# Performance work log

Measured on AMD Instinct MI355X. Metric: run time of the kernel, lower is better.

## Reference

```python
import jax, jax.numpy as jnp
import numpy as np

# LIFParameters(thr=0.4, tau=20.0, tau_o=20.0, damp=0.3, n_ref=5)
THR = 0.4
DECAY = float(np.exp(-1.0 / 20.0))   # membrane decay
KAPPA = float(np.exp(-1.0 / 20.0))   # output filter decay
N_REF = 5.0
DAMP = 0.3
SCALE = 1.0                           # scaling_factor

B, NIN, H, NOUT = 1024, 2048, 2048, 512


def setup_inputs() -> dict:
    key = jax.random.key(0)
    ks = jax.random.split(key, 10)
    inputs = (jax.random.uniform(ks[0], (B, NIN)) < 0.1).astype(jnp.float32)   # input spikes
    v = jax.random.uniform(ks[1], (B, H)) * THR                                # membrane potentials
    z = (jax.random.uniform(ks[2], (B, H)) < 0.2).astype(jnp.float32)          # previous spikes
    r = jax.random.randint(ks[3], (B, H), 0, 6).astype(jnp.float32)            # refractory counters
    out = jax.random.normal(ks[4], (B, NOUT)) * 0.1                            # filtered output
    trace_in = jax.random.uniform(ks[5], (B, NIN))
    trace_rec = jax.random.uniform(ks[6], (B, H))
    w_in = jax.random.normal(ks[7], (NIN, H)) / np.sqrt(NIN)
    w_rec = jax.random.normal(ks[8], (H, H)) / np.sqrt(H)
    w_out = jax.random.normal(ks[9], (H, NOUT)) / np.sqrt(H)
    return dict(inputs=inputs, v=v, z=z, r=r, out=out, trace_in=trace_in,
                trace_rec=trace_rec, w_in=w_in, w_rec=w_rec, w_out=w_out)


@jax.custom_vjp
def spike(v_scaled):
    return (v_scaled > 0.0).astype(v_scaled.dtype)

def _spike_fwd(v_scaled):
    return spike(v_scaled), v_scaled

def _spike_bwd(v_scaled, g):
    # surrogate gradient: damp * max(0, 1 - |v_scaled|)
    return (g * DAMP * jnp.maximum(1.0 - jnp.abs(v_scaled), 0.0),)

spike.defvjp(_spike_fwd, _spike_bwd)


def reference(inputs, v, z, r, out, trace_in, trace_rec, w_in, w_rec, w_out):
    # --- lif_step ---
    i_t = inputs @ w_in + z @ w_rec                      # [B,H] synaptic current
    new_v = DECAY * v + i_t - z * THR                    # leaky integration + reset
    v_scaled = (new_v - THR) / THR
    new_z = spike(v_scaled)
    new_z = jnp.where(r > 0.1, 0.0, new_z)               # refractory masking (old r)
    new_r = jnp.clip(r + N_REF * new_z - 1.0, 0.0, N_REF)
    new_out = KAPPA * out + new_z @ (w_out * SCALE)      # [B,NOUT]
    # --- e-prop extras (call_eprop) ---
    dz_dh = jnp.maximum(DAMP * (1.0 - jnp.abs(v_scaled)), 0.0) / THR
    dz_dh = jnp.where(r > 0.1, 0.0, dz_dh)               # zero in refractory period
    new_trace_in = trace_in * DECAY + inputs
    new_trace_rec = trace_rec * DECAY + z
    return (new_out, new_z, new_v, new_r, new_trace_in, new_trace_rec, dz_dh)
```

## Files before the change

### kernel.cpp

```cpp
#include <hip/hip_runtime.h>

#define Bq 1024
#define Hq 2048
#define NOUTq 512

#define DECAYF 0.95122942450071400910f
#define THRF 0.4f

#define OFF_OUT  0
#define OFF_Z    524288
#define OFF_V    2621440
#define OFF_R    4718592
#define OFF_TIN  6815744
#define OFF_TREC 8912896
#define OFF_DZ   11010048

#define WS_ACOMB 0ul
#define WS_WHI   8388608ul
#define WS_WLO   25165824ul
#define WS_WOUTT 41943040ul
#define WS_P     44040192ul
#define WS_Z2    77594624ul
#define WS_NEED  81788928ul

typedef __attribute__((ext_vector_type(8))) short  bf16x8;
typedef __attribute__((ext_vector_type(4))) short  s16x4;
typedef __attribute__((ext_vector_type(4))) float  f32x4;

__device__ __forceinline__ unsigned short cvt_bf16(float f) {
  unsigned u = __float_as_uint(f);
  return (unsigned short)((u + 0x7FFFu + ((u >> 16) & 1u)) >> 16);
}

__device__ __forceinline__ void gl_lds16(const void* g, void* l) {
  __builtin_amdgcn_global_load_lds((const __attribute__((address_space(1))) unsigned int*)g,
                                   (__attribute__((address_space(3))) unsigned int*)l, 16, 0, 0);
}


__global__ __launch_bounds__(256)
void prepWA(const float* __restrict__ w_in, const float* __restrict__ w_rec,
            const float* __restrict__ w_out, short* __restrict__ Whi,
            short* __restrict__ Wlo, short* __restrict__ WoutT,
            const f32x4* __restrict__ ins, const f32x4* __restrict__ zin,
            short* __restrict__ Acomb)
{
  __shared__ float tile[64][65];
  const int bx = blockIdx.x, tid = threadIdx.x;
  if (bx >= 2304) {
    const int i = (bx - 2304) * 256 + tid;
    const f32x4 b = ins[i];
    const f32x4 d = zin[i];
    const int e = i * 4, m = e >> 11, k = e & 2047;
    s16x4 ab, zb;
#pragma unroll
    for (int j = 0; j < 4; ++j) { ab[j] = (short)cvt_bf16(b[j]); zb[j] = (short)cvt_bf16(d[j]); }
    *(s16x4*)&Acomb[m * 4096 + k] = ab;
    *(s16x4*)&Acomb[m * 4096 + 2048 + k] = zb;
    return;
  }
  const int rr = tid >> 4, c4 = (tid & 15) * 4;
  if (bx < 2048) {
    const int k0 = (bx >> 5) * 64, n0 = (bx & 31) * 64;
#pragma unroll
    for (int p = 0; p < 4; ++p) {
      const int kk = p * 16 + rr, kg = k0 + kk;
      const float* src = (kg < 2048) ? &w_in[kg * 2048 + n0 + c4]
                                     : &w_rec[(kg - 2048) * 2048 + n0 + c4];
      const f32x4 v = *(const f32x4*)src;
#pragma unroll
      for (int j = 0; j < 4; ++j) tile[kk][c4 + j] = v[j];
    }
    __syncthreads();
#pragma unroll
    for (int p = 0; p < 4; ++p) {
      const int nn = p * 16 + rr;
      s16x4 hh, ll;
#pragma unroll
      for (int j = 0; j < 4; ++j) {
        const float w = tile[c4 + j][nn];
        const unsigned short h = cvt_bf16(w);
        hh[j] = (short)h;
        ll[j] = (short)cvt_bf16(w - __uint_as_float(((unsigned)h) << 16));
      }
      *(s16x4*)&Whi[(n0 + nn) * 4096 + k0 + c4] = hh;
      *(s16x4*)&Wlo[(n0 + nn) * 4096 + k0 + c4] = ll;
    }
  } else {
    const int b2 = bx - 2048;
    const int k0 = (b2 >> 3) * 64, n0 = (b2 & 7) * 64;
#pragma unroll
    for (int p = 0; p < 4; ++p) {
      const int kk = p * 16 + rr;
      const f32x4 v = *(const f32x4*)&w_out[(k0 + kk) * 512 + n0 + c4];
#pragma unroll
      for (int j = 0; j < 4; ++j) tile[kk][c4 + j] = v[j];
    }
    __syncthreads();
#pragma unroll
    for (int p = 0; p < 4; ++p) {
      const int nn = p * 16 + rr;
      s16x4 hh;
#pragma unroll
      for (int j = 0; j < 4; ++j) hh[j] = (short)cvt_bf16(tile[c4 + j][nn]);
      *(s16x4*)&WoutT[(n0 + nn) * 2048 + k0 + c4] = hh;
    }
  }
}

__global__ __launch_bounds__(256, 1)
void gemm1(const short* __restrict__ Ag, const short* __restrict__ Whg,
           const short* __restrict__ Wlg, float* __restrict__ outp)
{
  constexpr int BM = 128, BN = 128, MR = 4, NR = 4, KT = 16, AK = 4096;
  constexpr int APW = BM / 32, WPW = BN / 32;

  __shared__ __align__(16) short As[BM * 64];
  __shared__ __align__(16) short Wh[BN * 64];
  __shared__ __align__(16) short Wl[BN * 64];

  const int tid = threadIdx.x, lane = tid & 63, wv = tid >> 6;
  const int lr = lane & 15, hl = lane >> 4;
  const int rA = lane >> 3, ts = lane & 7;

  const int bid = blockIdx.x;
  const int swz = (bid & 7) * 64 + (bid >> 3);
  const int m0 = (swz & 7) * BM;
  const int n0 = ((swz >> 3) & 15) * BN;
  const int kz = swz >> 7;
  const int kb = kz * 1024;
  float* P = outp + (size_t)kz * (Bq * Hq);

  const int wm = (wv >> 1) * (MR * 16);
  const int wn = (wv & 1) * (NR * 16);

  f32x4 acc[MR][NR];
#pragma unroll
  for (int mi = 0; mi < MR; ++mi)
#pragma unroll
    for (int ni = 0; ni < NR; ++ni) acc[mi][ni] = (f32x4){0.f, 0.f, 0.f, 0.f};

  auto STAGE = [&](int kt) {
    const int k = kb + kt * 64;
#pragma unroll
    for (int q = 0; q < APW; ++q) {
      const int slot = wv * APW + q;
      const int r = slot * 8 + rA;
      const int s = ts ^ (r & 7);
      gl_lds16(Ag + (m0 + r) * AK + k + s * 8, &As[slot * 512]);
    }
#pragma unroll
    for (int q = 0; q < WPW; ++q) {
      const int slot = wv * WPW + q;
      const int r = slot * 8 + rA;
      const int s = ts ^ (r & 7);
      gl_lds16(Whg + (n0 + r) * AK + k + s * 8, &Wh[slot * 512]);
      gl_lds16(Wlg + (n0 + r) * AK + k + s * 8, &Wl[slot * 512]);
    }
  };

  STAGE(0);
  for (int kt = 0; kt < KT; ++kt) {
    __syncthreads();
#pragma unroll
    for (int ks = 0; ks < 2; ++ks) {
      bf16x8 af[MR];
#pragma unroll
      for (int mi = 0; mi < MR; ++mi) {
        const int r = wm + mi * 16 + lr;
        af[mi] = *(const bf16x8*)&As[r * 64 + (((ks * 4 + hl) ^ (r & 7)) << 3)];
      }
#pragma unroll
      for (int ni = 0; ni < NR; ++ni) {
        const int rn = wn + ni * 16 + lr;
        const int sp = (((ks * 4 + hl) ^ (rn & 7)) << 3);
        const bf16x8 bh = *(const bf16x8*)&Wh[rn * 64 + sp];
#pragma unroll
        for (int mi = 0; mi < MR; ++mi)
          acc[mi][ni] = __builtin_amdgcn_mfma_f32_16x16x32_bf16(af[mi], bh, acc[mi][ni], 0, 0, 0);
        const bf16x8 bl = *(const bf16x8*)&Wl[rn * 64 + sp];
#pragma unroll
        for (int mi = 0; mi < MR; ++mi)
          acc[mi][ni] = __builtin_amdgcn_mfma_f32_16x16x32_bf16(af[mi], bl, acc[mi][ni], 0, 0, 0);
      }
    }
    __syncthreads();
    if (kt + 1 < KT) STAGE(kt + 1);
  }

#pragma unroll
  for (int mi = 0; mi < MR; ++mi)
#pragma unroll
    for (int ni = 0; ni < NR; ++ni)
#pragma unroll
      for (int j = 0; j < 4; ++j) {
        const int m = m0 + wm + mi * 16 + hl * 4 + j;
        const int n = n0 + wn + ni * 16 + lr;
        P[m * Hq + n] = acc[mi][ni][j];
      }
}

__global__ __launch_bounds__(256)
void lif_epi(const f32x4* __restrict__ Pp, const f32x4* __restrict__ vin,
             const f32x4* __restrict__ zin, const f32x4* __restrict__ rin,
             float* __restrict__ dout, short* __restrict__ z2)
{
  const int i = blockIdx.x * 256 + threadIdx.x;
  const f32x4 it = Pp[i] + Pp[i + 524288] + Pp[i + 2 * 524288] + Pp[i + 3 * 524288];
  const f32x4 vo = vin[i], zo = zin[i], ro = rin[i];
  f32x4 nv, nz, nr, dz;
  s16x4 zb;
#pragma unroll
  for (int j = 0; j < 4; ++j) {
    const float v1 = DECAYF * vo[j] + it[j] - zo[j] * THRF;
    const float vs = (v1 - THRF) / THRF;
    const bool refr = ro[j] > 0.1f;
    const float z1 = (refr || !(vs > 0.0f)) ? 0.0f : 1.0f;
    nv[j] = v1; nz[j] = z1;
    nr[j] = fminf(fmaxf(ro[j] + 5.0f * z1 - 1.0f, 0.0f), 5.0f);
    dz[j] = refr ? 0.0f : (fmaxf(0.3f * (1.0f - fabsf(vs)), 0.0f) / THRF);
    zb[j] = (short)cvt_bf16(z1);
  }
  ((f32x4*)(dout + OFF_V))[i] = nv;
  ((f32x4*)(dout + OFF_Z))[i] = nz;
  ((f32x4*)(dout + OFF_R))[i] = nr;
  ((f32x4*)(dout + OFF_DZ))[i] = dz;
  ((s16x4*)z2)[i] = zb;
}

__global__ __launch_bounds__(256)
void tail(const short* __restrict__ Ag, const short* __restrict__ Whg,
          const float* __restrict__ e0, float* __restrict__ outp,
          const f32x4* __restrict__ tin, const f32x4* __restrict__ ins,
          const f32x4* __restrict__ trec, const f32x4* __restrict__ zin,
          f32x4* __restrict__ o1, f32x4* __restrict__ o2)
{
  constexpr int BM = 32, BN = 64, MR = 1, NR = 2, KT = 32, AK = 2048;
  constexpr int APW = BM / 32, WPW = BN / 32;
  __shared__ __align__(16) short As[BM * 64];
  __shared__ __align__(16) short Wh[BN * 64];

  const int bid = blockIdx.x, tid = threadIdx.x;
  if (bid >= 256) {
    const int i = (bid - 256) * 256 + tid;
    o1[i] = tin[i] * DECAYF + ins[i];
    o2[i] = trec[i] * DECAYF + zin[i];
    return;
  }
  const int lane = tid & 63, wv = tid >> 6;
  const int lr = lane & 15, hl = lane >> 4;
  const int rA = lane >> 3, ts = lane & 7;
  const int m0 = (bid >> 3) * BM, n0 = (bid & 7) * BN;
  const int wm = (wv >> 1) * (MR * 16);
  const int wn = (wv & 1) * (NR * 16);

  f32x4 acc[MR][NR];
#pragma unroll
  for (int mi = 0; mi < MR; ++mi)
#pragma unroll
    for (int ni = 0; ni < NR; ++ni) acc[mi][ni] = (f32x4){0.f, 0.f, 0.f, 0.f};

  auto STAGE = [&](int kt) {
    const int k = kt * 64;
#pragma unroll
    for (int q = 0; q < APW; ++q) {
      const int slot = wv * APW + q;
      const int r = slot * 8 + rA;
      const int s = ts ^ (r & 7);
      gl_lds16(Ag + (m0 + r) * AK + k + s * 8, &As[slot * 512]);
    }
#pragma unroll
    for (int q = 0; q < WPW; ++q) {
      const int slot = wv * WPW + q;
      const int r = slot * 8 + rA;
      const int s = ts ^ (r & 7);
      gl_lds16(Whg + (n0 + r) * AK + k + s * 8, &Wh[slot * 512]);
    }
  };

  STAGE(0);
  for (int kt = 0; kt < KT; ++kt) {
    __syncthreads();
#pragma unroll
    for (int ks = 0; ks < 2; ++ks) {
      bf16x8 af[MR];
#pragma unroll
      for (int mi = 0; mi < MR; ++mi) {
        const int r = wm + mi * 16 + lr;
        af[mi] = *(const bf16x8*)&As[r * 64 + (((ks * 4 + hl) ^ (r & 7)) << 3)];
      }
#pragma unroll
      for (int ni = 0; ni < NR; ++ni) {
        const int rn = wn + ni * 16 + lr;
        const int sp = (((ks * 4 + hl) ^ (rn & 7)) << 3);
        const bf16x8 bh = *(const bf16x8*)&Wh[rn * 64 + sp];
#pragma unroll
        for (int mi = 0; mi < MR; ++mi)
          acc[mi][ni] = __builtin_amdgcn_mfma_f32_16x16x32_bf16(af[mi], bh, acc[mi][ni], 0, 0, 0);
      }
    }
    __syncthreads();
    if (kt + 1 < KT) STAGE(kt + 1);
  }

#pragma unroll
  for (int mi = 0; mi < MR; ++mi)
#pragma unroll
    for (int ni = 0; ni < NR; ++ni)
#pragma unroll
      for (int j = 0; j < 4; ++j) {
        const int m = m0 + wm + mi * 16 + hl * 4 + j;
        const int n = n0 + wn + ni * 16 + lr;
        const int idx = m * NOUTq + n;
        outp[idx] = DECAYF * e0[idx] + acc[mi][ni][j];
      }
}


template<int MODE>
__global__ __launch_bounds__(256, 1)
void fb_gemm(const float* __restrict__ A0g, const float* __restrict__ A1g,
             const float* __restrict__ W0g, const float* __restrict__ W1g,
             const float* __restrict__ e0, const float* __restrict__ e1,
             const float* __restrict__ e2, float* __restrict__ dout)
{
  constexpr int BM = (MODE == 0) ? 64 : 32;
  constexpr int BN = (MODE == 0) ? 128 : 64;
  constexpr int BK = 64;
  constexpr int LDA = BK + 8;
  constexpr int MR = (MODE == 0) ? 2 : 1;
  constexpr int NR = (MODE == 0) ? 4 : 2;
  constexpr int WM = MR * 16, WN = NR * 16;
  constexpr int KT = (MODE == 0) ? 64 : 32;
  constexpr int Nmat = (MODE == 0) ? Hq : NOUTq;
  constexpr int QA = BM / 16;
  constexpr int QW = (16 * BN) / 256;
  constexpr int KSH = (MODE == 0) ? 7 : 6;
  constexpr int KSTEP = (MODE == 0) ? 2 : 4;

  __shared__ __align__(16) short As[BM * LDA];
  __shared__ __align__(16) short Wh[BN * LDA];
  __shared__ __align__(16) short Wl[((MODE == 0) ? BN : 1) * LDA];

  const int tid  = threadIdx.x;
  const int lane = tid & 63;
  const int wave = tid >> 6;
  const int lr = lane & 15, hl = lane >> 4;
  const int wmOff = (wave >> 1) * WM;
  const int wnOff = (wave & 1) * WN;
  const int m0 = blockIdx.y * BM;
  const int n0 = blockIdx.x * BN;
  const int arow = tid >> 4, ac4 = tid & 15;
  const int wn = tid & (BN - 1);

  f32x4 aR[QA];
  float wR[QW][4];
  f32x4 acc[MR][NR];
#pragma unroll
  for (int mi = 0; mi < MR; ++mi)
#pragma unroll
    for (int ni = 0; ni < NR; ++ni)
      acc[mi][ni] = (f32x4){0.f, 0.f, 0.f, 0.f};

  auto LOAD = [&](int kt) {
    const float* Ag = A0g; const float* Wg = W0g; int k0 = kt * BK;
    if (MODE == 0 && kt >= 32) { Ag = A1g; Wg = W1g; k0 = (kt - 32) * BK; }
#pragma unroll
    for (int q = 0; q < QA; ++q)
      aR[q] = *(const f32x4*)&Ag[(m0 + arow + q * 16) * 2048 + k0 + ac4 * 4];
#pragma unroll
    for (int p = 0; p < QW; ++p) {
      const int kq = (tid >> KSH) + p * KSTEP;
#pragma unroll
      for (int i = 0; i < 4; ++i)
        wR[p][i] = Wg[(k0 + kq * 4 + i) * Nmat + n0 + wn];
    }
  };

  auto STORE = [&]() {
#pragma unroll
    for (int q = 0; q < QA; ++q) {
      s16x4 hv;
#pragma unroll
      for (int j = 0; j < 4; ++j) hv[j] = (short)cvt_bf16(aR[q][j]);
      *(s16x4*)&As[(arow + q * 16) * LDA + ac4 * 4] = hv;
    }
#pragma unroll
    for (int p = 0; p < QW; ++p) {
      const int kq = (tid >> KSH) + p * KSTEP;
      s16x4 hh, ll;
#pragma unroll
      for (int i = 0; i < 4; ++i) {
        const float w = wR[p][i];
        const unsigned short h = cvt_bf16(w);
        hh[i] = (short)h;
        if (MODE == 0) {
          const float hf = __uint_as_float(((unsigned)h) << 16);
          ll[i] = (short)cvt_bf16(w - hf);
        }
      }
      *(s16x4*)&Wh[wn * LDA + kq * 4] = hh;
      if (MODE == 0) *(s16x4*)&Wl[wn * LDA + kq * 4] = ll;
    }
  };

  LOAD(0);
  for (int kt = 0; kt < KT; ++kt) {
    __syncthreads();
    STORE();
    __syncthreads();
    if (kt + 1 < KT) LOAD(kt + 1);
#pragma unroll
    for (int ks = 0; ks < 2; ++ks) {
      bf16x8 af[MR];
#pragma unroll
      for (int mi = 0; mi < MR; ++mi)
        af[mi] = *(const bf16x8*)&As[(wmOff + mi * 16 + lr) * LDA + ks * 32 + hl * 8];
#pragma unroll
      for (int ni = 0; ni < NR; ++ni) {
        const bf16x8 bh = *(const bf16x8*)&Wh[(wnOff + ni * 16 + lr) * LDA + ks * 32 + hl * 8];
#pragma unroll
        for (int mi = 0; mi < MR; ++mi)
          acc[mi][ni] = __builtin_amdgcn_mfma_f32_16x16x32_bf16(af[mi], bh, acc[mi][ni], 0, 0, 0);
        if (MODE == 0) {
          const bf16x8 bl = *(const bf16x8*)&Wl[(wnOff + ni * 16 + lr) * LDA + ks * 32 + hl * 8];
#pragma unroll
          for (int mi = 0; mi < MR; ++mi)
            acc[mi][ni] = __builtin_amdgcn_mfma_f32_16x16x32_bf16(af[mi], bl, acc[mi][ni], 0, 0, 0);
        }
      }
    }
  }

#pragma unroll
  for (int mi = 0; mi < MR; ++mi) {
#pragma unroll
    for (int ni = 0; ni < NR; ++ni) {
#pragma unroll
      for (int j = 0; j < 4; ++j) {
        const int m = m0 + wmOff + mi * 16 + hl * 4 + j;
        const int n = n0 + wnOff + ni * 16 + lr;
        if (MODE == 0) {
          const int idx = m * Hq + n;
          const float it = acc[mi][ni][j];
          const float vold = e0[idx];
          const float zold = e1[idx];
          const float rold = e2[idx];
          const float nv = DECAYF * vold + it - zold * THRF;
          const float vs = (nv - THRF) / THRF;
          const bool refr = rold > 0.1f;
          const float nz = (refr || !(vs > 0.0f)) ? 0.0f : 1.0f;
          const float nr = fminf(fmaxf(rold + 5.0f * nz - 1.0f, 0.0f), 5.0f);
          const float dz = refr ? 0.0f : (fmaxf(0.3f * (1.0f - fabsf(vs)), 0.0f) / THRF);
          dout[OFF_V + idx] = nv;
          dout[OFF_Z + idx] = nz;
          dout[OFF_R + idx] = nr;
          dout[OFF_DZ + idx] = dz;
        } else {
          const int idx = m * NOUTq + n;
          dout[OFF_OUT + idx] = DECAYF * e0[idx] + acc[mi][ni][j];
        }
      }
    }
  }
}

__global__ __launch_bounds__(256)
void fb_trace(const float4* __restrict__ tin, const float4* __restrict__ ins,
              const float4* __restrict__ trec, const float4* __restrict__ zin,
              float4* __restrict__ o1, float4* __restrict__ o2)
{
  const int n4 = (Bq * 2048) / 4;
  for (int i = blockIdx.x * blockDim.x + threadIdx.x; i < n4; i += gridDim.x * blockDim.x) {
    const float4 a = tin[i], b = ins[i];
    float4 u;
    u.x = a.x * DECAYF + b.x; u.y = a.y * DECAYF + b.y;
    u.z = a.z * DECAYF + b.z; u.w = a.w * DECAYF + b.w;
    o1[i] = u;
    const float4 c = trec[i], d = zin[i];
    float4 w;
    w.x = c.x * DECAYF + d.x; w.y = c.y * DECAYF + d.y;
    w.z = c.z * DECAYF + d.z; w.w = c.w * DECAYF + d.w;
    o2[i] = w;
  }
}

extern "C" void kernel_launch(void* const* d_in, const int* in_sizes, int n_in,
                              void* d_out, int out_size, void* d_ws, size_t ws_size,
                              hipStream_t stream) {
  const float* inputs = (const float*)d_in[0];
  const float* v      = (const float*)d_in[1];
  const float* z      = (const float*)d_in[2];
  const float* r      = (const float*)d_in[3];
  const float* outp   = (const float*)d_in[4];
  const float* tin    = (const float*)d_in[5];
  const float* trec   = (const float*)d_in[6];
  const float* w_in   = (const float*)d_in[7];
  const float* w_rec  = (const float*)d_in[8];
  const float* w_out  = (const float*)d_in[9];
  float* out = (float*)d_out;

  if (ws_size >= WS_NEED) {
    char* ws = (char*)d_ws;
    short* Acomb = (short*)(ws + WS_ACOMB);
    short* Whi   = (short*)(ws + WS_WHI);
    short* Wlo   = (short*)(ws + WS_WLO);
    short* WoutT = (short*)(ws + WS_WOUTT);
    float* P     = (float*)(ws + WS_P);
    short* Z2    = (short*)(ws + WS_Z2);

    prepWA<<<4352, 256, 0, stream>>>(w_in, w_rec, w_out, Whi, Wlo, WoutT,
                                     (const f32x4*)inputs, (const f32x4*)z, Acomb);
    gemm1<<<512, 256, 0, stream>>>(Acomb, Whi, Wlo, P);
    lif_epi<<<2048, 256, 0, stream>>>((const f32x4*)P, (const f32x4*)v, (const f32x4*)z,
                                      (const f32x4*)r, out, Z2);
    tail<<<2304, 256, 0, stream>>>(Z2, WoutT, outp, out + OFF_OUT,
                                   (const f32x4*)tin, (const f32x4*)inputs,
                                   (const f32x4*)trec, (const f32x4*)z,
                                   (f32x4*)(out + OFF_TIN), (f32x4*)(out + OFF_TREC));
  } else {
    fb_trace<<<2048, 256, 0, stream>>>((const float4*)tin, (const float4*)inputs,
                                       (const float4*)trec, (const float4*)z,
                                       (float4*)(out + OFF_TIN), (float4*)(out + OFF_TREC));
    fb_gemm<0><<<dim3(16, 16), 256, 0, stream>>>(inputs, z, w_in, w_rec, v, z, r, out);
    fb_gemm<1><<<dim3(8, 32), 256, 0, stream>>>(out + OFF_Z, nullptr, w_out, nullptr,
                                                outp, nullptr, nullptr, out);
  }
}
```

Measured before the change: 91.23 us.

## Replace bf16 hi/lo split GEMM with three-limb int8 fixed-point GEMM

Weights are quantized to a 21-bit fixed-point integer split into three signed 7-bit limbs. Spike inputs are stored as 0/1 int8. The main GEMM then uses int8 MFMA (16x16x64) with int32 accumulators, and the partial sums are recombined with shifts. The epilogue rescales the integer K-split partials back to float. The goal is to halve A-operand bytes, cut weight bytes, and use the higher int8 matrix throughput. In exchange it adds a third accumulator set, which raises register pressure, and a fixed-point quantization error on the weights.

```diff
diff --git a/kernel.cpp b/kernel.cpp
--- a/kernel.cpp
+++ b/kernel.cpp
@@ -6,6 +6,7 @@
 
 #define DECAYF 0.95122942450071400910f
 #define THRF 0.4f
+#define SINVF 5931641.0f
 
 #define OFF_OUT  0
 #define OFF_Z    524288
@@ -15,17 +16,20 @@
 #define OFF_TREC 8912896
 #define OFF_DZ   11010048
 
-#define WS_ACOMB 0ul
-#define WS_WHI   8388608ul
-#define WS_WLO   25165824ul
-#define WS_WOUTT 41943040ul
-#define WS_P     44040192ul
-#define WS_Z2    77594624ul
-#define WS_NEED  81788928ul
+#define WS_A     0ul
+#define WS_Q0    4194304ul
+#define WS_Q1    12582912ul
+#define WS_Q2    20971520ul
+#define WS_WOUTT 29360128ul
+#define WS_P     31457280ul
+#define WS_Z2    65011712ul
+#define WS_NEED  69206016ul
 
 typedef __attribute__((ext_vector_type(8))) short  bf16x8;
 typedef __attribute__((ext_vector_type(4))) short  s16x4;
 typedef __attribute__((ext_vector_type(4))) float  f32x4;
+typedef __attribute__((ext_vector_type(4))) int    i32x4;
+typedef __attribute__((ext_vector_type(4))) char   c8x4;
 
 __device__ __forceinline__ unsigned short cvt_bf16(float f) {
   unsigned u = __float_as_uint(f);
@@ -39,11 +43,12 @@
 
 
 __global__ __launch_bounds__(256)
-void prepWA(const float* __restrict__ w_in, const float* __restrict__ w_rec,
-            const float* __restrict__ w_out, short* __restrict__ Whi,
-            short* __restrict__ Wlo, short* __restrict__ WoutT,
-            const f32x4* __restrict__ ins, const f32x4* __restrict__ zin,
-            short* __restrict__ Acomb)
+void prep(const float* __restrict__ w_in, const float* __restrict__ w_rec,
+          const float* __restrict__ w_out, signed char* __restrict__ Q0,
+          signed char* __restrict__ Q1, signed char* __restrict__ Q2,
+          short* __restrict__ WoutT,
+          const f32x4* __restrict__ ins, const f32x4* __restrict__ zin,
+          signed char* __restrict__ Acomb)
 {
   __shared__ float tile[64][65];
   const int bx = blockIdx.x, tid = threadIdx.x;
@@ -52,11 +57,11 @@
     const f32x4 b = ins[i];
     const f32x4 d = zin[i];
     const int e = i * 4, m = e >> 11, k = e & 2047;
-    s16x4 ab, zb;
-#pragma unroll
-    for (int j = 0; j < 4; ++j) { ab[j] = (short)cvt_bf16(b[j]); zb[j] = (short)cvt_bf16(d[j]); }
-    *(s16x4*)&Acomb[m * 4096 + k] = ab;
-    *(s16x4*)&Acomb[m * 4096 + 2048 + k] = zb;
+    c8x4 ab, zb;
+#pragma unroll
+    for (int j = 0; j < 4; ++j) { ab[j] = (char)(b[j] != 0.0f); zb[j] = (char)(d[j] != 0.0f); }
+    *(c8x4*)&Acomb[m * 4096 + k] = ab;
+    *(c8x4*)&Acomb[m * 4096 + 2048 + k] = zb;
     return;
   }
   const int rr = tid >> 4, c4 = (tid & 15) * 4;
@@ -75,16 +80,18 @@
 #pragma unroll
     for (int p = 0; p < 4; ++p) {
       const int nn = p * 16 + rr;
-      s16x4 hh, ll;
+      c8x4 b0, b1, b2;
 #pragma unroll
       for (int j = 0; j < 4; ++j) {
-        const float w = tile[c4 + j][nn];
-        const unsigned short h = cvt_bf16(w);
-        hh[j] = (short)h;
-        ll[j] = (short)cvt_bf16(w - __uint_as_float(((unsigned)h) << 16));
-      }
-      *(s16x4*)&Whi[(n0 + nn) * 4096 + k0 + c4] = hh;
-      *(s16x4*)&Wlo[(n0 + nn) * 4096 + k0 + c4] = ll;
+        int q = __float2int_rn(tile[c4 + j][nn] * SINVF);
+        const int d2 = ((q + 64) & 127) - 64;  q = (q - d2) >> 7;
+        const int d1 = ((q + 64) & 127) - 64;  q = (q - d1) >> 7;
+        b2[j] = (char)d2; b1[j] = (char)d1; b0[j] = (char)q;
+      }
+      const long off = (long)(n0 + nn) * 4096 + k0 + c4;
+      *(c8x4*)&Q0[off] = b0;
+      *(c8x4*)&Q1[off] = b1;
+      *(c8x4*)&Q2[off] = b2;
     }
   } else {
     const int b2 = bx - 2048;
@@ -108,54 +115,53 @@
   }
 }
 
-__global__ __launch_bounds__(256, 1)
-void gemm1(const short* __restrict__ Ag, const short* __restrict__ Whg,
-           const short* __restrict__ Wlg, float* __restrict__ outp)
+__global__ __launch_bounds__(256, 2)
+void gemm1(const signed char* __restrict__ Ag, const signed char* __restrict__ Q0g,
+           const signed char* __restrict__ Q1g, const signed char* __restrict__ Q2g,
+           int* __restrict__ outp)
 {
-  constexpr int BM = 128, BN = 128, MR = 4, NR = 4, KT = 16, AK = 4096;
-  constexpr int APW = BM / 32, WPW = BN / 32;
-
-  __shared__ __align__(16) short As[BM * 64];
-  __shared__ __align__(16) short Wh[BN * 64];
-  __shared__ __align__(16) short Wl[BN * 64];
+  constexpr int KT = 8;
+  __shared__ __align__(16) signed char As[128 * 128];
+  __shared__ __align__(16) signed char B0[128 * 128];
+  __shared__ __align__(16) signed char B1[128 * 128];
+  __shared__ __align__(16) signed char B2[128 * 128];
 
   const int tid = threadIdx.x, lane = tid & 63, wv = tid >> 6;
   const int lr = lane & 15, hl = lane >> 4;
-  const int rA = lane >> 3, ts = lane & 7;
+  const int r8 = lane >> 3, ts = lane & 7;
 
   const int bid = blockIdx.x;
   const int swz = (bid & 7) * 64 + (bid >> 3);
-  const int m0 = (swz & 7) * BM;
-  const int n0 = ((swz >> 3) & 15) * BN;
+  const int m0 = (swz & 7) * 128;
+  const int n0 = ((swz >> 3) & 15) * 128;
   const int kz = swz >> 7;
   const int kb = kz * 1024;
-  float* P = outp + (size_t)kz * (Bq * Hq);
-
-  const int wm = (wv >> 1) * (MR * 16);
-  const int wn = (wv & 1) * (NR * 16);
-
-  f32x4 acc[MR][NR];
-#pragma unroll
-  for (int mi = 0; mi < MR; ++mi)
-#pragma unroll
-    for (int ni = 0; ni < NR; ++ni) acc[mi][ni] = (f32x4){0.f, 0.f, 0.f, 0.f};
+  int* P = outp + (size_t)kz * (Bq * Hq);
+
+  const int wm = (wv >> 1) * 64;
+  const int wn = (wv & 1) * 64;
+
+  i32x4 a0[4][4], a1[4][4], a2[4][4];
+#pragma unroll
+  for (int mi = 0; mi < 4; ++mi)
+#pragma unroll
+    for (int ni = 0; ni < 4; ++ni) {
+      a0[mi][ni] = (i32x4){0, 0, 0, 0};
+      a1[mi][ni] = (i32x4){0, 0, 0, 0};
+      a2[mi][ni] = (i32x4){0, 0, 0, 0};
+    }
 
   auto STAGE = [&](int kt) {
-    const int k = kb + kt * 64;
-#pragma unroll
-    for (int q = 0; q < APW; ++q) {
-      const int slot = wv * APW + q;
-      const int r = slot * 8 + rA;
+    const int k = kb + kt * 128;
+#pragma unroll
+    for (int q = 0; q < 4; ++q) {
+      const int slot = wv * 4 + q;
+      const int r = slot * 8 + r8;
       const int s = ts ^ (r & 7);
-      gl_lds16(Ag + (m0 + r) * AK + k + s * 8, &As[slot * 512]);
-    }
-#pragma unroll
-    for (int q = 0; q < WPW; ++q) {
-      const int slot = wv * WPW + q;
-      const int r = slot * 8 + rA;
-      const int s = ts ^ (r & 7);
-      gl_lds16(Whg + (n0 + r) * AK + k + s * 8, &Wh[slot * 512]);
-      gl_lds16(Wlg + (n0 + r) * AK + k + s * 8, &Wl[slot * 512]);
+      gl_lds16(Ag + (size_t)(m0 + r) * 4096 + k + s * 16, &As[slot * 1024]);
+      gl_lds16(Q0g + (size_t)(n0 + r) * 4096 + k + s * 16, &B0[slot * 1024]);
+      gl_lds16(Q1g + (size_t)(n0 + r) * 4096 + k + s * 16, &B1[slot * 1024]);
+      gl_lds16(Q2g + (size_t)(n0 + r) * 4096 + k + s * 16, &B2[slot * 1024]);
     }
   };
 
@@ -164,24 +170,28 @@
     __syncthreads();
 #pragma unroll
     for (int ks = 0; ks < 2; ++ks) {
-      bf16x8 af[MR];
-#pragma unroll
-      for (int mi = 0; mi < MR; ++mi) {
-        const int r = wm + mi * 16 + lr;
-        af[mi] = *(const bf16x8*)&As[r * 64 + (((ks * 4 + hl) ^ (r & 7)) << 3)];
-      }
-#pragma unroll
-      for (int ni = 0; ni < NR; ++ni) {
-        const int rn = wn + ni * 16 + lr;
-        const int sp = (((ks * 4 + hl) ^ (rn & 7)) << 3);
-        const bf16x8 bh = *(const bf16x8*)&Wh[rn * 64 + sp];
-#pragma unroll
-        for (int mi = 0; mi < MR; ++mi)
-          acc[mi][ni] = __builtin_amdgcn_mfma_f32_16x16x32_bf16(af[mi], bh, acc[mi][ni], 0, 0, 0);
-        const bf16x8 bl = *(const bf16x8*)&Wl[rn * 64 + sp];
-#pragma unroll
-        for (int mi = 0; mi < MR; ++mi)
-          acc[mi][ni] = __builtin_amdgcn_mfma_f32_16x16x32_bf16(af[mi], bl, acc[mi][ni], 0, 0, 0);
+      i32x4 af[4];
+#pragma unroll
+      for (int mi = 0; mi < 4; ++mi) {
+        const int ar = wm + mi * 16 + lr;
+        af[mi] = *(const i32x4*)&As[ar * 128 + (((ks * 4 + hl) ^ (ar & 7)) << 4)];
+      }
+#pragma unroll
+      for (int ni = 0; ni < 4; ++ni) {
+        const int br = wn + ni * 16 + lr;
+        const int sp = (((ks * 4 + hl) ^ (br & 7)) << 4);
+        const i32x4 b0 = *(const i32x4*)&B0[br * 128 + sp];
+#pragma unroll
+        for (int mi = 0; mi < 4; ++mi)
+          a0[mi][ni] = __builtin_amdgcn_mfma_i32_16x16x64_i8(af[mi], b0, a0[mi][ni], 0, 0, 0);
+        const i32x4 b1 = *(const i32x4*)&B1[br * 128 + sp];
+#pragma unroll
+        for (int mi = 0; mi < 4; ++mi)
+          a1[mi][ni] = __builtin_amdgcn_mfma_i32_16x16x64_i8(af[mi], b1, a1[mi][ni], 0, 0, 0);
+        const i32x4 b2 = *(const i32x4*)&B2[br * 128 + sp];
+#pragma unroll
+        for (int mi = 0; mi < 4; ++mi)
+          a2[mi][ni] = __builtin_amdgcn_mfma_i32_16x16x64_i8(af[mi], b2, a2[mi][ni], 0, 0, 0);
       }
     }
     __syncthreads();
@@ -189,30 +199,32 @@
   }
 
 #pragma unroll
-  for (int mi = 0; mi < MR; ++mi)
-#pragma unroll
-    for (int ni = 0; ni < NR; ++ni)
+  for (int mi = 0; mi < 4; ++mi)
+#pragma unroll
+    for (int ni = 0; ni < 4; ++ni)
 #pragma unroll
       for (int j = 0; j < 4; ++j) {
         const int m = m0 + wm + mi * 16 + hl * 4 + j;
         const int n = n0 + wn + ni * 16 + lr;
-        P[m * Hq + n] = acc[mi][ni][j];
+        P[m * Hq + n] = (a0[mi][ni][j] << 14) + (a1[mi][ni][j] << 7) + a2[mi][ni][j];
       }
 }
 
 __global__ __launch_bounds__(256)
-void lif_epi(const f32x4* __restrict__ Pp, const f32x4* __restrict__ vin,
+void lif_epi(const i32x4* __restrict__ Pp, const f32x4* __restrict__ vin,
              const f32x4* __restrict__ zin, const f32x4* __restrict__ rin,
              float* __restrict__ dout, short* __restrict__ z2)
 {
   const int i = blockIdx.x * 256 + threadIdx.x;
-  const f32x4 it = Pp[i] + Pp[i + 524288] + Pp[i + 2 * 524288] + Pp[i + 3 * 524288];
+  const i32x4 c = Pp[i] + Pp[i + 524288] + Pp[i + 2 * 524288] + Pp[i + 3 * 524288];
+  const double S = 1.0 / (double)SINVF;
   const f32x4 vo = vin[i], zo = zin[i], ro = rin[i];
   f32x4 nv, nz, nr, dz;
   s16x4 zb;
 #pragma unroll
   for (int j = 0; j < 4; ++j) {
-    const float v1 = DECAYF * vo[j] + it[j] - zo[j] * THRF;
+    const float it = (float)((double)c[j] * S);
+    const float v1 = DECAYF * vo[j] + it - zo[j] * THRF;
     const float vs = (v1 - THRF) / THRF;
     const bool refr = ro[j] > 0.1f;
     const float z1 = (refr || !(vs > 0.0f)) ? 0.0f : 1.0f;
@@ -502,17 +514,18 @@
 
   if (ws_size >= WS_NEED) {
     char* ws = (char*)d_ws;
-    short* Acomb = (short*)(ws + WS_ACOMB);
-    short* Whi   = (short*)(ws + WS_WHI);
-    short* Wlo   = (short*)(ws + WS_WLO);
-    short* WoutT = (short*)(ws + WS_WOUTT);
-    float* P     = (float*)(ws + WS_P);
-    short* Z2    = (short*)(ws + WS_Z2);
-
-    prepWA<<<4352, 256, 0, stream>>>(w_in, w_rec, w_out, Whi, Wlo, WoutT,
-                                     (const f32x4*)inputs, (const f32x4*)z, Acomb);
-    gemm1<<<512, 256, 0, stream>>>(Acomb, Whi, Wlo, P);
-    lif_epi<<<2048, 256, 0, stream>>>((const f32x4*)P, (const f32x4*)v, (const f32x4*)z,
+    signed char* A  = (signed char*)(ws + WS_A);
+    signed char* Q0 = (signed char*)(ws + WS_Q0);
+    signed char* Q1 = (signed char*)(ws + WS_Q1);
+    signed char* Q2 = (signed char*)(ws + WS_Q2);
+    short* WoutT    = (short*)(ws + WS_WOUTT);
+    int* P          = (int*)(ws + WS_P);
+    short* Z2       = (short*)(ws + WS_Z2);
+
+    prep<<<4352, 256, 0, stream>>>(w_in, w_rec, w_out, Q0, Q1, Q2, WoutT,
+                                   (const f32x4*)inputs, (const f32x4*)z, A);
+    gemm1<<<512, 256, 0, stream>>>(A, Q0, Q1, Q2, P);
+    lif_epi<<<2048, 256, 0, stream>>>((const i32x4*)P, (const f32x4*)v, (const f32x4*)z,
                                       (const f32x4*)r, out, Z2);
     tail<<<2304, 256, 0, stream>>>(Z2, WoutT, outp, out + OFF_OUT,
                                    (const f32x4*)tin, (const f32x4*)inputs,
```

After: 88.85 us. 1.03x faster.
